# Kernel tuning notes

Measured on AMD Instinct MI355X. Metric: run time of the kernel, lower is better.

## Reference

```python
import jax, jax.numpy as jnp
import numpy as np

GAMMA = 0.9865


def setup_inputs() -> dict:
    key = jax.random.key(0)
    ks = jax.random.split(key, 6)
    B, T, DIN, D = 8, 2048, 1024, 1024
    return {
        "xq": jax.random.normal(ks[0], (B, T, DIN), dtype=jnp.float32),
        "xk": jax.random.normal(ks[1], (B, T, DIN), dtype=jnp.float32),
        "xv": jax.random.normal(ks[2], (B, T, DIN), dtype=jnp.float32),
        "Wq": jax.random.normal(ks[3], (DIN, D), dtype=jnp.float32) * (DIN ** -0.5),
        "Wk": jax.random.normal(ks[4], (DIN, D), dtype=jnp.float32) * (DIN ** -0.5),
        "Wv": jax.random.normal(ks[5], (DIN, D), dtype=jnp.float32) * (DIN ** -0.5),
    }


def reference(xq, xk, xv, Wq, Wk, Wv):
    # Dense projections (no bias)
    Q = jnp.einsum("btd,de->bte", xq, Wq)  # [B,T,D]
    K = jnp.einsum("btd,de->bte", xk, Wk)
    V = jnp.einsum("btd,de->bte", xv, Wv)

    # einsum('ib,bj->bj', K_t^T, V_t) == (sum_i K[b,t,i]) * V[b,t,:]
    ksum = jnp.sum(K, axis=-1)            # [B,T]
    u = ksum[..., None] * V               # [B,T,D]
    # recurrence starts at t=1 with s[0]=0, so u[0] never contributes
    u = u * (jnp.arange(u.shape[1]) > 0)[None, :, None]

    def step(s, u_t):
        s = s * jnp.float32(GAMMA) + u_t
        return s, s

    s0 = jnp.zeros(u.shape[::2], dtype=u.dtype)          # [B,D]
    _, S = jax.lax.scan(step, s0, jnp.swapaxes(u, 0, 1))  # S: [T,B,D]
    return Q * jnp.swapaxes(S, 0, 1)                      # [B,T,D]
```

## Files before the change

kernel.cpp:

```cpp
#include <hip/hip_runtime.h>
#include <hip/hip_bf16.h>

#define GAMMA 0.9865f

typedef __attribute__((ext_vector_type(8))) short bf16x8;
typedef __attribute__((ext_vector_type(4))) float f32x4;

static constexpr int Bb  = 8;
static constexpr int Tt  = 2048;
static constexpr int DIN = 1024;
static constexpr int Dd  = 1024;
static constexpr int Mm  = Bb * Tt;
static constexpr int CL  = 64;
static constexpr int NC  = Tt / CL;
static constexpr int NT  = DIN / 64;

__device__ __forceinline__ void gload16(const void* g, void* l) {
  __builtin_amdgcn_global_load_lds(
      (const __attribute__((address_space(1))) void*)g,
      (__attribute__((address_space(3))) void*)l, 16, 0, 0);
}

__device__ __forceinline__ void bar() {
  asm volatile("" ::: "memory");
  __builtin_amdgcn_s_barrier();
  asm volatile("" ::: "memory");
}

__global__ void wsum_kernel(const float* __restrict__ Wk, float* __restrict__ wsum) {
  int row  = blockIdx.x * 4 + (threadIdx.x >> 6);
  int lane = threadIdx.x & 63;
  const float4* rp = (const float4*)(Wk + (size_t)row * DIN);
  float s = 0.f;
#pragma unroll
  for (int i = 0; i < 4; ++i) {
    float4 v = rp[lane + i * 64];
    s += v.x + v.y + v.z + v.w;
  }
  for (int off = 32; off; off >>= 1) s += __shfl_down(s, off);
  if (lane == 0) wsum[row] = s;
}

__global__ void wt_kernel(const float* __restrict__ Wq, const float* __restrict__ Wv,
                          __hip_bfloat16* __restrict__ Wt) {
  const float* W = blockIdx.z ? Wv : Wq;
  __hip_bfloat16* outp = Wt + (size_t)blockIdx.z * DIN * Dd;
  __shared__ float tile[32][33];
  int k0 = blockIdx.x * 32, n0 = blockIdx.y * 32;
  int tx = threadIdx.x, ty = threadIdx.y;
#pragma unroll
  for (int i = 0; i < 4; ++i)
    tile[ty + i * 8][tx] = W[(size_t)(k0 + ty + i * 8) * Dd + n0 + tx];
  __syncthreads();
#pragma unroll
  for (int i = 0; i < 4; ++i)
    outp[(size_t)(n0 + ty + i * 8) * DIN + k0 + tx] =
        __float2bfloat16(tile[tx][ty + i * 8]);
}

__global__ __launch_bounds__(256) void cast_kernel(
    const float* __restrict__ xq, const float* __restrict__ xv,
    __hip_bfloat16* __restrict__ oq, __hip_bfloat16* __restrict__ ov) {
  const float* src = blockIdx.y ? xv : xq;
  __hip_bfloat16* dst = blockIdx.y ? ov : oq;
  size_t i = (size_t)blockIdx.x * 256 + threadIdx.x;
  const float4* p = (const float4*)src;
  float4 a = p[i * 2], b = p[i * 2 + 1];
  union { __hip_bfloat16 h[8]; bf16x8 v; } u;
  u.h[0] = __float2bfloat16(a.x); u.h[1] = __float2bfloat16(a.y);
  u.h[2] = __float2bfloat16(a.z); u.h[3] = __float2bfloat16(a.w);
  u.h[4] = __float2bfloat16(b.x); u.h[5] = __float2bfloat16(b.y);
  u.h[6] = __float2bfloat16(b.z); u.h[7] = __float2bfloat16(b.w);
  ((bf16x8*)dst)[i] = u.v;
}


__device__ __forceinline__ void stage_half(const __hip_bfloat16* g, char* l, int tid) {
#pragma unroll
  for (int j = 0; j < 2; ++j) {
    int c = tid + j * 512;
    int row = c >> 3, ch = c & 7;
    gload16(g + (size_t)row * DIN + ((ch ^ (row & 7)) << 3), l + c * 16);
  }
}

__device__ __forceinline__ bf16x8 lds_frag(const char* base, int row, int kc) {
  return *(const bf16x8*)(base + (((row << 3) + (kc ^ (row & 7))) << 4));
}

#define MFMA_QUAD(MLO, NLO)                                                  \
  _Pragma("unroll") for (int mi = 0; mi < 4; ++mi)                           \
  _Pragma("unroll") for (int ni = 0; ni < 2; ++ni)                           \
  _Pragma("unroll") for (int ks = 0; ks < 2; ++ks)                           \
      acc[(MLO) + mi][(NLO) + ni] = __builtin_amdgcn_mfma_f32_16x16x32_bf16( \
          a[(MLO) + mi][ks], b[(NLO) + ni][ks], acc[(MLO) + mi][(NLO) + ni], 0, 0, 0);

__global__ __launch_bounds__(512, 2) void gemm8_kernel(
    const __hip_bfloat16* __restrict__ Aq, const __hip_bfloat16* __restrict__ Av,
    const __hip_bfloat16* __restrict__ Wt,
    __hip_bfloat16* __restrict__ Qbf, __hip_bfloat16* __restrict__ Vbf) {
  extern __shared__ char lds[];

  int lin = blockIdx.x;
  int wg  = (lin & 7) * 64 + (lin >> 3);
  int z   = wg >> 8, rem = wg & 255;
  int by  = rem & 3, bx = rem >> 2;

  const __hip_bfloat16* Ab = z ? Av : Aq;
  const int m0 = bx * 256, n0 = by * 256;
  const __hip_bfloat16* Ag = Ab + (size_t)m0 * DIN;
  const __hip_bfloat16* Bg = Wt + ((size_t)z * Dd + n0) * DIN;
  __hip_bfloat16* Cc = z ? Vbf : Qbf;

  const int tid = threadIdx.x;
  const int wv = tid >> 6, lane = tid & 63;
  const int wm = (wv >> 2) * 128, wn = (wv & 3) * 64;
  const int fq = lane >> 4, fr = lane & 15;

  f32x4 acc[8][4] = {};

  stage_half(Ag,                  lds,                 tid);
  stage_half(Ag + 128 * DIN,      lds + 16384,         tid);
  stage_half(Bg,                  lds + 32768,         tid);
  stage_half(Bg + 128 * DIN,      lds + 49152,         tid);
  stage_half(Ag + 64,             lds + 65536,         tid);
  stage_half(Ag + 128 * DIN + 64, lds + 65536 + 16384, tid);
  asm volatile("s_waitcnt vmcnt(4)" ::: "memory");
  bar();

  for (int t = 0; t < NT; ++t) {
    char* buf  = lds + (t & 1) * 65536;
    char* bufN = lds + ((t + 1) & 1) * 65536;
    const char* At = buf;
    const char* Bt = buf + 32768;
    bf16x8 a[8][2], b[4][2];

#pragma unroll
    for (int mi = 0; mi < 4; ++mi)
#pragma unroll
      for (int ks = 0; ks < 2; ++ks)
        a[mi][ks] = lds_frag(At, wm + mi * 16 + fr, ks * 4 + fq);
#pragma unroll
    for (int ni = 0; ni < 2; ++ni)
#pragma unroll
      for (int ks = 0; ks < 2; ++ks)
        b[ni][ks] = lds_frag(Bt, wn + ni * 16 + fr, ks * 4 + fq);
    if (t + 1 < NT) stage_half(Bg + (size_t)(t + 1) * 64, bufN + 32768, tid);
    bar();
    __builtin_amdgcn_s_setprio(1);
    MFMA_QUAD(0, 0);
    __builtin_amdgcn_s_setprio(0);
    bar();

#pragma unroll
    for (int mi = 4; mi < 8; ++mi)
#pragma unroll
      for (int ks = 0; ks < 2; ++ks)
        a[mi][ks] = lds_frag(At, wm + mi * 16 + fr, ks * 4 + fq);
    if (t + 1 < NT)
      stage_half(Bg + 128 * DIN + (size_t)(t + 1) * 64, bufN + 49152, tid);
    bar();
    __builtin_amdgcn_s_setprio(1);
    MFMA_QUAD(4, 0);
    __builtin_amdgcn_s_setprio(0);
    bar();

#pragma unroll
    for (int ni = 2; ni < 4; ++ni)
#pragma unroll
      for (int ks = 0; ks < 2; ++ks)
        b[ni][ks] = lds_frag(Bt, wn + ni * 16 + fr, ks * 4 + fq);
    if (t + 2 < NT) stage_half(Ag + (size_t)(t + 2) * 64, buf, tid);
    bar();
    __builtin_amdgcn_s_setprio(1);
    MFMA_QUAD(0, 2);
    __builtin_amdgcn_s_setprio(0);
    bar();

    if (t + 2 < NT)
      stage_half(Ag + 128 * DIN + (size_t)(t + 2) * 64, buf + 16384, tid);
    if (t + 1 < NT) {
      if (t + 2 < NT) asm volatile("s_waitcnt vmcnt(4)" ::: "memory");
      else            asm volatile("s_waitcnt vmcnt(0)" ::: "memory");
    }
    bar();
    __builtin_amdgcn_s_setprio(1);
    MFMA_QUAD(4, 2);
    __builtin_amdgcn_s_setprio(0);
    bar();
  }

#pragma unroll
  for (int mi = 0; mi < 8; ++mi) {
#pragma unroll
    for (int ni = 0; ni < 4; ++ni) {
      f32x4 v = acc[mi][ni];
      int row = m0 + wm + mi * 16 + fq * 4;
      int col = n0 + wn + ni * 16 + fr;
#pragma unroll
      for (int j = 0; j < 4; ++j)
        Cc[(size_t)(row + j) * Dd + col] = __float2bfloat16(v[j]);
    }
  }
}

__global__ void ksum_kernel(const float* __restrict__ xk, const float* __restrict__ wsum,
                            float* __restrict__ ksum) {
  int row  = blockIdx.x * 4 + (threadIdx.x >> 6);
  int lane = threadIdx.x & 63;
  const float4* rp = (const float4*)(xk + (size_t)row * DIN);
  const float4* wp = (const float4*)wsum;
  float s = 0.f;
#pragma unroll
  for (int i = 0; i < 4; ++i) {
    float4 a = rp[lane + i * 64];
    float4 w = wp[lane + i * 64];
    s += a.x * w.x + a.y * w.y + a.z * w.z + a.w * w.w;
  }
  for (int off = 32; off; off >>= 1) s += __shfl_down(s, off);
  if (lane == 0) ksum[row] = s;
}

__global__ void scanA_kernel(const __hip_bfloat16* __restrict__ Vbf,
                             const float* __restrict__ ksum,
                             float* __restrict__ E) {
  int b = blockIdx.x, c = blockIdx.y;
  int d = blockIdx.z * 256 + threadIdx.x;
  const __hip_bfloat16* Vp = Vbf + ((size_t)(b * Tt + c * CL) * Dd) + d;
  const float* kp = ksum + b * Tt + c * CL;
  float s = 0.f;
#pragma unroll 8
  for (int t = 0; t < CL; ++t) {
    float u = kp[t] * __bfloat162float(Vp[(size_t)t * Dd]);
    if (c == 0 && t == 0) u = 0.f;
    s = s * GAMMA + u;
  }
  E[((size_t)b * NC + c) * Dd + d] = s;
}

__global__ void scanB_kernel(const float* __restrict__ E, float* __restrict__ carry,
                             float gCL) {
  int b = blockIdx.x;
  int d = blockIdx.y * 256 + threadIdx.x;
  float send = 0.f;
  for (int c = 0; c < NC; ++c) {
    size_t idx = ((size_t)b * NC + c) * Dd + d;
    float e = E[idx];
    carry[idx] = send;
    send = e + gCL * send;
  }
}

__global__ void final_kernel(const __hip_bfloat16* __restrict__ Vbf,
                             const __hip_bfloat16* __restrict__ Qbf,
                             const float* __restrict__ ksum,
                             const float* __restrict__ carry,
                             float* __restrict__ outp) {
  int b = blockIdx.x, c = blockIdx.y;
  int d = blockIdx.z * 256 + threadIdx.x;
  size_t base = ((size_t)(b * Tt + c * CL) * Dd) + d;
  float s = carry[((size_t)b * NC + c) * Dd + d];
  const float* kp = ksum + b * Tt + c * CL;
#pragma unroll 4
  for (int t = 0; t < CL; ++t) {
    float u = kp[t] * __bfloat162float(Vbf[base + (size_t)t * Dd]);
    if (c == 0 && t == 0) u = 0.f;
    s = s * GAMMA + u;
    outp[base + (size_t)t * Dd] = __bfloat162float(Qbf[base + (size_t)t * Dd]) * s;
  }
}

extern "C" void kernel_launch(void* const* d_in, const int* in_sizes, int n_in,
                              void* d_out, int out_size, void* d_ws, size_t ws_size,
                              hipStream_t stream) {
  (void)in_sizes; (void)n_in; (void)out_size; (void)ws_size;
  const float* xq = (const float*)d_in[0];
  const float* xk = (const float*)d_in[1];
  const float* xv = (const float*)d_in[2];
  const float* Wq = (const float*)d_in[3];
  const float* Wk = (const float*)d_in[4];
  const float* Wv = (const float*)d_in[5];
  float* outp = (float*)d_out;

  char* ws = (char*)d_ws;
  size_t off = 0;
  auto alloc = [&](size_t bytes) {
    char* p = ws + off;
    off += (bytes + 255) & ~(size_t)255;
    return p;
  };
  __hip_bfloat16* xq_bf = (__hip_bfloat16*)alloc((size_t)Mm * DIN * 2);
  __hip_bfloat16* xv_bf = (__hip_bfloat16*)alloc((size_t)Mm * DIN * 2);
  __hip_bfloat16* Wt    = (__hip_bfloat16*)alloc((size_t)2 * DIN * Dd * 2);
  __hip_bfloat16* Qbf   = (__hip_bfloat16*)alloc((size_t)Mm * Dd * 2);
  __hip_bfloat16* Vbf   = (__hip_bfloat16*)alloc((size_t)Mm * Dd * 2);
  float* wsum  = (float*)alloc((size_t)DIN * 4);
  float* ksum  = (float*)alloc((size_t)Mm * 4);
  float* E     = (float*)alloc((size_t)Bb * NC * Dd * 4);
  float* carry = (float*)alloc((size_t)Bb * NC * Dd * 4);

  double g = 1.0;
  for (int i = 0; i < CL; ++i) g *= (double)GAMMA;
  float gCL = (float)g;

  (void)hipFuncSetAttribute((const void*)gemm8_kernel,
                            hipFuncAttributeMaxDynamicSharedMemorySize, 131072);

  wsum_kernel<<<DIN / 4, 256, 0, stream>>>(Wk, wsum);
  wt_kernel<<<dim3(DIN / 32, Dd / 32, 2), dim3(32, 8), 0, stream>>>(Wq, Wv, Wt);
  cast_kernel<<<dim3(Mm * DIN / 8 / 256, 2), 256, 0, stream>>>(xq, xv, xq_bf, xv_bf);
  ksum_kernel<<<Mm / 4, 256, 0, stream>>>(xk, wsum, ksum);
  gemm8_kernel<<<512, 512, 131072, stream>>>(xq_bf, xv_bf, Wt, Qbf, Vbf);
  scanA_kernel<<<dim3(Bb, NC, Dd / 256), 256, 0, stream>>>(Vbf, ksum, E);
  scanB_kernel<<<dim3(Bb, Dd / 256), 256, 0, stream>>>(E, carry, gCL);
  final_kernel<<<dim3(Bb, NC, Dd / 256), 256, 0, stream>>>(Vbf, Qbf, ksum, carry, outp);
}
```

Measured before the change: 157.0 us.

## Fuse chunked scan stages into one cooperative kernel and merge weight prep kernels

Replaces the three scan kernels (chunk reduce, carry propagation, final apply) with a single cooperative kernel that uses grid-wide syncs. Each thread now handles two adjacent columns and keeps its 64 V values in registers, so V is read only once. Also merges the Wk row-sum and the weight transpose/cast into one launch. The aim is to cut launch overhead and the second V read, at the cost of 64 extra registers per thread and two grid barriers. The carry phase runs on only 4096 threads while the rest of the grid waits.

Result: slower. 236.0 us (+50.3%).

```diff
diff --git a/kernel.cpp b/kernel.cpp
--- a/kernel.cpp
+++ b/kernel.cpp
@@ -1,5 +1,6 @@
 #include <hip/hip_runtime.h>
 #include <hip/hip_bf16.h>
+#include <hip/hip_cooperative_groups.h>
 
 #define GAMMA 0.9865f
 
@@ -27,27 +28,40 @@
   asm volatile("" ::: "memory");
 }
 
-__global__ void wsum_kernel(const float* __restrict__ Wk, float* __restrict__ wsum) {
-  int row  = blockIdx.x * 4 + (threadIdx.x >> 6);
-  int lane = threadIdx.x & 63;
-  const float4* rp = (const float4*)(Wk + (size_t)row * DIN);
-  float s = 0.f;
-#pragma unroll
-  for (int i = 0; i < 4; ++i) {
-    float4 v = rp[lane + i * 64];
-    s += v.x + v.y + v.z + v.w;
-  }
-  for (int off = 32; off; off >>= 1) s += __shfl_down(s, off);
-  if (lane == 0) wsum[row] = s;
-}
-
-__global__ void wt_kernel(const float* __restrict__ Wq, const float* __restrict__ Wv,
-                          __hip_bfloat16* __restrict__ Wt) {
-  const float* W = blockIdx.z ? Wv : Wq;
-  __hip_bfloat16* outp = Wt + (size_t)blockIdx.z * DIN * Dd;
+__device__ __forceinline__ float bflo(unsigned int u) {
+  return __uint_as_float((u & 0xffffu) << 16);
+}
+__device__ __forceinline__ float bfhi(unsigned int u) {
+  return __uint_as_float(u & 0xffff0000u);
+}
+
+__global__ __launch_bounds__(256) void prep_kernel(
+    const float* __restrict__ Wq, const float* __restrict__ Wk,
+    const float* __restrict__ Wv, float* __restrict__ wsum,
+    __hip_bfloat16* __restrict__ Wt) {
+  int bid = blockIdx.x;
+  if (bid < 256) {
+    int row  = bid * 4 + (threadIdx.x >> 6);
+    int lane = threadIdx.x & 63;
+    const float4* rp = (const float4*)(Wk + (size_t)row * DIN);
+    float s = 0.f;
+#pragma unroll
+    for (int i = 0; i < 4; ++i) {
+      float4 v = rp[lane + i * 64];
+      s += v.x + v.y + v.z + v.w;
+    }
+    for (int off = 32; off; off >>= 1) s += __shfl_down(s, off);
+    if (lane == 0) wsum[row] = s;
+    return;
+  }
+  int wid = bid - 256;
+  int z = wid >> 10, rem = wid & 1023;
+  int kb = rem & 31, nb = rem >> 5;
+  const float* W = z ? Wv : Wq;
+  __hip_bfloat16* outp = Wt + (size_t)z * DIN * Dd;
   __shared__ float tile[32][33];
-  int k0 = blockIdx.x * 32, n0 = blockIdx.y * 32;
-  int tx = threadIdx.x, ty = threadIdx.y;
+  int k0 = kb * 32, n0 = nb * 32;
+  int tx = threadIdx.x & 31, ty = threadIdx.x >> 5;
 #pragma unroll
   for (int i = 0; i < 4; ++i)
     tile[ty + i * 8][tx] = W[(size_t)(k0 + ty + i * 8) * Dd + n0 + tx];
@@ -74,7 +88,6 @@
   ((bf16x8*)dst)[i] = u.v;
 }
 
-
 __device__ __forceinline__ void stage_half(const __hip_bfloat16* g, char* l, int tid) {
 #pragma unroll
   for (int j = 0; j < 2; ++j) {
@@ -221,52 +234,59 @@
   if (lane == 0) ksum[row] = s;
 }
 
-__global__ void scanA_kernel(const __hip_bfloat16* __restrict__ Vbf,
-                             const float* __restrict__ ksum,
-                             float* __restrict__ E) {
-  int b = blockIdx.x, c = blockIdx.y;
-  int d = blockIdx.z * 256 + threadIdx.x;
-  const __hip_bfloat16* Vp = Vbf + ((size_t)(b * Tt + c * CL) * Dd) + d;
+__global__ __launch_bounds__(512) void scanfused_kernel(
+    const __hip_bfloat16* __restrict__ Vbf, const __hip_bfloat16* __restrict__ Qbf,
+    const float* __restrict__ ksum, float2* __restrict__ E2,
+    float2* __restrict__ carry2, float gCL, float* __restrict__ outp) {
+  cooperative_groups::grid_group grid = cooperative_groups::this_grid();
+  int id = blockIdx.x * 512 + threadIdx.x;
+  int d2 = id & 511, c = (id >> 9) & 31, b = id >> 14;
+  const unsigned int* Vw = (const unsigned int*)Vbf;
+  size_t base = ((size_t)(b * Tt + c * CL)) * 512 + d2;
   const float* kp = ksum + b * Tt + c * CL;
-  float s = 0.f;
-#pragma unroll 8
+
+  unsigned int vs[64];
+  float s0 = 0.f, s1 = 0.f;
+#pragma unroll
   for (int t = 0; t < CL; ++t) {
-    float u = kp[t] * __bfloat162float(Vp[(size_t)t * Dd]);
-    if (c == 0 && t == 0) u = 0.f;
-    s = s * GAMMA + u;
-  }
-  E[((size_t)b * NC + c) * Dd + d] = s;
-}
-
-__global__ void scanB_kernel(const float* __restrict__ E, float* __restrict__ carry,
-                             float gCL) {
-  int b = blockIdx.x;
-  int d = blockIdx.y * 256 + threadIdx.x;
-  float send = 0.f;
-  for (int c = 0; c < NC; ++c) {
-    size_t idx = ((size_t)b * NC + c) * Dd + d;
-    float e = E[idx];
-    carry[idx] = send;
-    send = e + gCL * send;
-  }
-}
-
-__global__ void final_kernel(const __hip_bfloat16* __restrict__ Vbf,
-                             const __hip_bfloat16* __restrict__ Qbf,
-                             const float* __restrict__ ksum,
-                             const float* __restrict__ carry,
-                             float* __restrict__ outp) {
-  int b = blockIdx.x, c = blockIdx.y;
-  int d = blockIdx.z * 256 + threadIdx.x;
-  size_t base = ((size_t)(b * Tt + c * CL) * Dd) + d;
-  float s = carry[((size_t)b * NC + c) * Dd + d];
-  const float* kp = ksum + b * Tt + c * CL;
-#pragma unroll 4
+    unsigned int w = Vw[base + (size_t)t * 512];
+    vs[t] = w;
+    float kv = kp[t];
+    if (c == 0 && t == 0) kv = 0.f;
+    s0 = s0 * GAMMA + kv * bflo(w);
+    s1 = s1 * GAMMA + kv * bfhi(w);
+  }
+  E2[((size_t)b * NC + c) * 512 + d2] = make_float2(s0, s1);
+
+  grid.sync();
+
+  if (id < 4096) {
+    int bb = id >> 9, dd = id & 511;
+    float t0 = 0.f, t1 = 0.f;
+    for (int cc = 0; cc < NC; ++cc) {
+      size_t ix = ((size_t)bb * NC + cc) * 512 + dd;
+      float2 e = E2[ix];
+      carry2[ix] = make_float2(t0, t1);
+      t0 = e.x + gCL * t0;
+      t1 = e.y + gCL * t1;
+    }
+  }
+
+  grid.sync();
+
+  float2 cr = carry2[((size_t)b * NC + c) * 512 + d2];
+  s0 = cr.x; s1 = cr.y;
+  const unsigned int* Qw = (const unsigned int*)Qbf;
+  float2* Ow = (float2*)outp;
+#pragma unroll
   for (int t = 0; t < CL; ++t) {
-    float u = kp[t] * __bfloat162float(Vbf[base + (size_t)t * Dd]);
-    if (c == 0 && t == 0) u = 0.f;
-    s = s * GAMMA + u;
-    outp[base + (size_t)t * Dd] = __bfloat162float(Qbf[base + (size_t)t * Dd]) * s;
+    unsigned int w = vs[t];
+    float kv = kp[t];
+    if (c == 0 && t == 0) kv = 0.f;
+    s0 = s0 * GAMMA + kv * bflo(w);
+    s1 = s1 * GAMMA + kv * bfhi(w);
+    unsigned int qw = Qw[base + (size_t)t * 512];
+    Ow[base + (size_t)t * 512] = make_float2(bflo(qw) * s0, bfhi(qw) * s1);
   }
 }
 
@@ -294,10 +314,10 @@
   __hip_bfloat16* Wt    = (__hip_bfloat16*)alloc((size_t)2 * DIN * Dd * 2);
   __hip_bfloat16* Qbf   = (__hip_bfloat16*)alloc((size_t)Mm * Dd * 2);
   __hip_bfloat16* Vbf   = (__hip_bfloat16*)alloc((size_t)Mm * Dd * 2);
-  float* wsum  = (float*)alloc((size_t)DIN * 4);
-  float* ksum  = (float*)alloc((size_t)Mm * 4);
-  float* E     = (float*)alloc((size_t)Bb * NC * Dd * 4);
-  float* carry = (float*)alloc((size_t)Bb * NC * Dd * 4);
+  float* wsum   = (float*)alloc((size_t)DIN * 4);
+  float* ksum   = (float*)alloc((size_t)Mm * 4);
+  float2* E2    = (float2*)alloc((size_t)Bb * NC * 512 * 8);
+  float2* carry2= (float2*)alloc((size_t)Bb * NC * 512 * 8);
 
   double g = 1.0;
   for (int i = 0; i < CL; ++i) g *= (double)GAMMA;
@@ -306,12 +326,15 @@
   (void)hipFuncSetAttribute((const void*)gemm8_kernel,
                             hipFuncAttributeMaxDynamicSharedMemorySize, 131072);
 
-  wsum_kernel<<<DIN / 4, 256, 0, stream>>>(Wk, wsum);
-  wt_kernel<<<dim3(DIN / 32, Dd / 32, 2), dim3(32, 8), 0, stream>>>(Wq, Wv, Wt);
+  prep_kernel<<<256 + 2048, 256, 0, stream>>>(Wq, Wk, Wv, wsum, Wt);
   cast_kernel<<<dim3(Mm * DIN / 8 / 256, 2), 256, 0, stream>>>(xq, xv, xq_bf, xv_bf);
   ksum_kernel<<<Mm / 4, 256, 0, stream>>>(xk, wsum, ksum);
   gemm8_kernel<<<512, 512, 131072, stream>>>(xq_bf, xv_bf, Wt, Qbf, Vbf);
-  scanA_kernel<<<dim3(Bb, NC, Dd / 256), 256, 0, stream>>>(Vbf, ksum, E);
-  scanB_kernel<<<dim3(Bb, Dd / 256), 256, 0, stream>>>(E, carry, gCL);
-  final_kernel<<<dim3(Bb, NC, Dd / 256), 256, 0, stream>>>(Vbf, Qbf, ksum, carry, outp);
-}
+
+  const __hip_bfloat16* Vc = Vbf; const __hip_bfloat16* Qc = Qbf;
+  const float* kc = ksum;
+  void* cargs[] = { (void*)&Vc, (void*)&Qc, (void*)&kc, (void*)&E2,
+                    (void*)&carry2, (void*)&gCL, (void*)&outp };
+  (void)hipLaunchCooperativeKernel((const void*)scanfused_kernel,
+                                   dim3(256), dim3(512), cargs, 0, stream);
+}
```

## Fuse prep kernels and make GEMM blocks process two M tiles persistently

Applied to the files above, without the earlier changes.

The weight-sum and weight-transpose kernels are merged into one launch, and the activation cast is merged with the ksum reduction via an extra grid row. The GEMM launches 256 blocks instead of 512, and each block loops over two consecutive 256-row M tiles with the same B columns, re-staging the prologue between them. The aim is to cut launch overhead and get a single wave of blocks on the device. The cost is a serialized prologue and epilogue inside each block, plus a larger castksum grid in which many ksum blocks exit immediately.

New measurement: 173.2 us. 10.3% more time.

```diff
diff --git a/kernel.cpp b/kernel.cpp
--- a/kernel.cpp
+++ b/kernel.cpp
@@ -27,27 +27,33 @@
   asm volatile("" ::: "memory");
 }
 
-__global__ void wsum_kernel(const float* __restrict__ Wk, float* __restrict__ wsum) {
-  int row  = blockIdx.x * 4 + (threadIdx.x >> 6);
-  int lane = threadIdx.x & 63;
-  const float4* rp = (const float4*)(Wk + (size_t)row * DIN);
-  float s = 0.f;
-#pragma unroll
-  for (int i = 0; i < 4; ++i) {
-    float4 v = rp[lane + i * 64];
-    s += v.x + v.y + v.z + v.w;
-  }
-  for (int off = 32; off; off >>= 1) s += __shfl_down(s, off);
-  if (lane == 0) wsum[row] = s;
-}
-
-__global__ void wt_kernel(const float* __restrict__ Wq, const float* __restrict__ Wv,
-                          __hip_bfloat16* __restrict__ Wt) {
-  const float* W = blockIdx.z ? Wv : Wq;
-  __hip_bfloat16* outp = Wt + (size_t)blockIdx.z * DIN * Dd;
+__global__ __launch_bounds__(256) void prep_kernel(
+    const float* __restrict__ Wq, const float* __restrict__ Wk,
+    const float* __restrict__ Wv, float* __restrict__ wsum,
+    __hip_bfloat16* __restrict__ Wt) {
+  int bid = blockIdx.x;
+  if (bid < 256) {
+    int row  = bid * 4 + (threadIdx.x >> 6);
+    int lane = threadIdx.x & 63;
+    const float4* rp = (const float4*)(Wk + (size_t)row * DIN);
+    float s = 0.f;
+#pragma unroll
+    for (int i = 0; i < 4; ++i) {
+      float4 v = rp[lane + i * 64];
+      s += v.x + v.y + v.z + v.w;
+    }
+    for (int off = 32; off; off >>= 1) s += __shfl_down(s, off);
+    if (lane == 0) wsum[row] = s;
+    return;
+  }
+  int wid = bid - 256;
+  int z = wid >> 10, rem = wid & 1023;
+  int kb = rem & 31, nb = rem >> 5;
+  const float* W = z ? Wv : Wq;
+  __hip_bfloat16* outp = Wt + (size_t)z * DIN * Dd;
   __shared__ float tile[32][33];
-  int k0 = blockIdx.x * 32, n0 = blockIdx.y * 32;
-  int tx = threadIdx.x, ty = threadIdx.y;
+  int k0 = kb * 32, n0 = nb * 32;
+  int tx = threadIdx.x & 31, ty = threadIdx.x >> 5;
 #pragma unroll
   for (int i = 0; i < 4; ++i)
     tile[ty + i * 8][tx] = W[(size_t)(k0 + ty + i * 8) * Dd + n0 + tx];
@@ -58,20 +64,40 @@
         __float2bfloat16(tile[tx][ty + i * 8]);
 }
 
-__global__ __launch_bounds__(256) void cast_kernel(
-    const float* __restrict__ xq, const float* __restrict__ xv,
-    __hip_bfloat16* __restrict__ oq, __hip_bfloat16* __restrict__ ov) {
-  const float* src = blockIdx.y ? xv : xq;
-  __hip_bfloat16* dst = blockIdx.y ? ov : oq;
-  size_t i = (size_t)blockIdx.x * 256 + threadIdx.x;
-  const float4* p = (const float4*)src;
-  float4 a = p[i * 2], b = p[i * 2 + 1];
-  union { __hip_bfloat16 h[8]; bf16x8 v; } u;
-  u.h[0] = __float2bfloat16(a.x); u.h[1] = __float2bfloat16(a.y);
-  u.h[2] = __float2bfloat16(a.z); u.h[3] = __float2bfloat16(a.w);
-  u.h[4] = __float2bfloat16(b.x); u.h[5] = __float2bfloat16(b.y);
-  u.h[6] = __float2bfloat16(b.z); u.h[7] = __float2bfloat16(b.w);
-  ((bf16x8*)dst)[i] = u.v;
+__global__ __launch_bounds__(256) void castksum_kernel(
+    const float* __restrict__ xq, const float* __restrict__ xk,
+    const float* __restrict__ xv, const float* __restrict__ wsum,
+    __hip_bfloat16* __restrict__ oq, __hip_bfloat16* __restrict__ ov,
+    float* __restrict__ ksum) {
+  int y = blockIdx.y;
+  if (y < 2) {
+    const float* src = y ? xv : xq;
+    __hip_bfloat16* dst = y ? ov : oq;
+    size_t i = (size_t)blockIdx.x * 256 + threadIdx.x;
+    const float4* p = (const float4*)src;
+    float4 a = p[i * 2], b = p[i * 2 + 1];
+    union { __hip_bfloat16 h[8]; bf16x8 v; } u;
+    u.h[0] = __float2bfloat16(a.x); u.h[1] = __float2bfloat16(a.y);
+    u.h[2] = __float2bfloat16(a.z); u.h[3] = __float2bfloat16(a.w);
+    u.h[4] = __float2bfloat16(b.x); u.h[5] = __float2bfloat16(b.y);
+    u.h[6] = __float2bfloat16(b.z); u.h[7] = __float2bfloat16(b.w);
+    ((bf16x8*)dst)[i] = u.v;
+    return;
+  }
+  if (blockIdx.x >= Mm / 4) return;
+  int row  = blockIdx.x * 4 + (threadIdx.x >> 6);
+  int lane = threadIdx.x & 63;
+  const float4* rp = (const float4*)(xk + (size_t)row * DIN);
+  const float4* wp = (const float4*)wsum;
+  float s = 0.f;
+#pragma unroll
+  for (int i = 0; i < 4; ++i) {
+    float4 a = rp[lane + i * 64];
+    float4 w = wp[lane + i * 64];
+    s += a.x * w.x + a.y * w.y + a.z * w.z + a.w * w.w;
+  }
+  for (int off = 32; off; off >>= 1) s += __shfl_down(s, off);
+  if (lane == 0) ksum[row] = s;
 }
 
 
@@ -102,13 +128,12 @@
   extern __shared__ char lds[];
 
   int lin = blockIdx.x;
-  int wg  = (lin & 7) * 64 + (lin >> 3);
-  int z   = wg >> 8, rem = wg & 255;
-  int by  = rem & 3, bx = rem >> 2;
+  int wg  = (lin & 7) * 32 + (lin >> 3);
+  int z   = wg >> 7, rem = wg & 127;
+  int by  = rem & 3, bxp = rem >> 2;
 
   const __hip_bfloat16* Ab = z ? Av : Aq;
-  const int m0 = bx * 256, n0 = by * 256;
-  const __hip_bfloat16* Ag = Ab + (size_t)m0 * DIN;
+  const int n0 = by * 256;
   const __hip_bfloat16* Bg = Wt + ((size_t)z * Dd + n0) * DIN;
   __hip_bfloat16* Cc = z ? Vbf : Qbf;
 
@@ -117,108 +142,110 @@
   const int wm = (wv >> 2) * 128, wn = (wv & 3) * 64;
   const int fq = lane >> 4, fr = lane & 15;
 
-  f32x4 acc[8][4] = {};
-
-  stage_half(Ag,                  lds,                 tid);
-  stage_half(Ag + 128 * DIN,      lds + 16384,         tid);
-  stage_half(Bg,                  lds + 32768,         tid);
-  stage_half(Bg + 128 * DIN,      lds + 49152,         tid);
-  stage_half(Ag + 64,             lds + 65536,         tid);
-  stage_half(Ag + 128 * DIN + 64, lds + 65536 + 16384, tid);
-  asm volatile("s_waitcnt vmcnt(4)" ::: "memory");
-  bar();
-
-  for (int t = 0; t < NT; ++t) {
-    char* buf  = lds + (t & 1) * 65536;
-    char* bufN = lds + ((t + 1) & 1) * 65536;
-    const char* At = buf;
-    const char* Bt = buf + 32768;
-    bf16x8 a[8][2], b[4][2];
-
-#pragma unroll
-    for (int mi = 0; mi < 4; ++mi)
-#pragma unroll
-      for (int ks = 0; ks < 2; ++ks)
-        a[mi][ks] = lds_frag(At, wm + mi * 16 + fr, ks * 4 + fq);
-#pragma unroll
-    for (int ni = 0; ni < 2; ++ni)
-#pragma unroll
-      for (int ks = 0; ks < 2; ++ks)
-        b[ni][ks] = lds_frag(Bt, wn + ni * 16 + fr, ks * 4 + fq);
-    if (t + 1 < NT) stage_half(Bg + (size_t)(t + 1) * 64, bufN + 32768, tid);
+  {
+    const __hip_bfloat16* Ag = Ab + (size_t)(bxp * 2) * 256 * DIN;
+    stage_half(Ag,                  lds,                 tid);
+    stage_half(Ag + 128 * DIN,      lds + 16384,         tid);
+    stage_half(Bg,                  lds + 32768,         tid);
+    stage_half(Bg + 128 * DIN,      lds + 49152,         tid);
+    stage_half(Ag + 64,             lds + 65536,         tid);
+    stage_half(Ag + 128 * DIN + 64, lds + 65536 + 16384, tid);
+    asm volatile("s_waitcnt vmcnt(4)" ::: "memory");
     bar();
-    __builtin_amdgcn_s_setprio(1);
-    MFMA_QUAD(0, 0);
-    __builtin_amdgcn_s_setprio(0);
-    bar();
-
-#pragma unroll
-    for (int mi = 4; mi < 8; ++mi)
-#pragma unroll
-      for (int ks = 0; ks < 2; ++ks)
-        a[mi][ks] = lds_frag(At, wm + mi * 16 + fr, ks * 4 + fq);
-    if (t + 1 < NT)
-      stage_half(Bg + 128 * DIN + (size_t)(t + 1) * 64, bufN + 49152, tid);
-    bar();
-    __builtin_amdgcn_s_setprio(1);
-    MFMA_QUAD(4, 0);
-    __builtin_amdgcn_s_setprio(0);
-    bar();
-
-#pragma unroll
-    for (int ni = 2; ni < 4; ++ni)
-#pragma unroll
-      for (int ks = 0; ks < 2; ++ks)
-        b[ni][ks] = lds_frag(Bt, wn + ni * 16 + fr, ks * 4 + fq);
-    if (t + 2 < NT) stage_half(Ag + (size_t)(t + 2) * 64, buf, tid);
-    bar();
-    __builtin_amdgcn_s_setprio(1);
-    MFMA_QUAD(0, 2);
-    __builtin_amdgcn_s_setprio(0);
-    bar();
-
-    if (t + 2 < NT)
-      stage_half(Ag + 128 * DIN + (size_t)(t + 2) * 64, buf + 16384, tid);
-    if (t + 1 < NT) {
-      if (t + 2 < NT) asm volatile("s_waitcnt vmcnt(4)" ::: "memory");
-      else            asm volatile("s_waitcnt vmcnt(0)" ::: "memory");
+  }
+
+  for (int rep = 0; rep < 2; ++rep) {
+    const int m0 = (bxp * 2 + rep) * 256;
+    const __hip_bfloat16* Ag = Ab + (size_t)m0 * DIN;
+    f32x4 acc[8][4] = {};
+
+    for (int t = 0; t < NT; ++t) {
+      char* buf  = lds + (t & 1) * 65536;
+      char* bufN = lds + ((t + 1) & 1) * 65536;
+      const char* At = buf;
+      const char* Bt = buf + 32768;
+      bf16x8 a[8][2], b[4][2];
+
+#pragma unroll
+      for (int mi = 0; mi < 4; ++mi)
+#pragma unroll
+        for (int ks = 0; ks < 2; ++ks)
+          a[mi][ks] = lds_frag(At, wm + mi * 16 + fr, ks * 4 + fq);
+#pragma unroll
+      for (int ni = 0; ni < 2; ++ni)
+#pragma unroll
+        for (int ks = 0; ks < 2; ++ks)
+          b[ni][ks] = lds_frag(Bt, wn + ni * 16 + fr, ks * 4 + fq);
+      if (t + 1 < NT) stage_half(Bg + (size_t)(t + 1) * 64, bufN + 32768, tid);
+      bar();
+      __builtin_amdgcn_s_setprio(1);
+      MFMA_QUAD(0, 0);
+      __builtin_amdgcn_s_setprio(0);
+      bar();
+
+#pragma unroll
+      for (int mi = 4; mi < 8; ++mi)
+#pragma unroll
+        for (int ks = 0; ks < 2; ++ks)
+          a[mi][ks] = lds_frag(At, wm + mi * 16 + fr, ks * 4 + fq);
+      if (t + 1 < NT)
+        stage_half(Bg + 128 * DIN + (size_t)(t + 1) * 64, bufN + 49152, tid);
+      bar();
+      __builtin_amdgcn_s_setprio(1);
+      MFMA_QUAD(4, 0);
+      __builtin_amdgcn_s_setprio(0);
+      bar();
+
+#pragma unroll
+      for (int ni = 2; ni < 4; ++ni)
+#pragma unroll
+        for (int ks = 0; ks < 2; ++ks)
+          b[ni][ks] = lds_frag(Bt, wn + ni * 16 + fr, ks * 4 + fq);
+      if (t + 2 < NT) stage_half(Ag + (size_t)(t + 2) * 64, buf, tid);
+      bar();
+      __builtin_amdgcn_s_setprio(1);
+      MFMA_QUAD(0, 2);
+      __builtin_amdgcn_s_setprio(0);
+      bar();
+
+      if (t + 2 < NT)
+        stage_half(Ag + 128 * DIN + (size_t)(t + 2) * 64, buf + 16384, tid);
+      if (t + 1 < NT) {
+        if (t + 2 < NT) asm volatile("s_waitcnt vmcnt(4)" ::: "memory");
+        else            asm volatile("s_waitcnt vmcnt(0)" ::: "memory");
+      }
+      bar();
+      __builtin_amdgcn_s_setprio(1);
+      MFMA_QUAD(4, 2);
+      __builtin_amdgcn_s_setprio(0);
+      bar();
     }
-    bar();
-    __builtin_amdgcn_s_setprio(1);
-    MFMA_QUAD(4, 2);
-    __builtin_amdgcn_s_setprio(0);
-    bar();
-  }
-
-#pragma unroll
-  for (int mi = 0; mi < 8; ++mi) {
-#pragma unroll
-    for (int ni = 0; ni < 4; ++ni) {
-      f32x4 v = acc[mi][ni];
-      int row = m0 + wm + mi * 16 + fq * 4;
-      int col = n0 + wn + ni * 16 + fr;
-#pragma unroll
-      for (int j = 0; j < 4; ++j)
-        Cc[(size_t)(row + j) * Dd + col] = __float2bfloat16(v[j]);
+
+#pragma unroll
+    for (int mi = 0; mi < 8; ++mi) {
+#pragma unroll
+      for (int ni = 0; ni < 4; ++ni) {
+        f32x4 v = acc[mi][ni];
+        int row = m0 + wm + mi * 16 + fq * 4;
+        int col = n0 + wn + ni * 16 + fr;
+#pragma unroll
+        for (int j = 0; j < 4; ++j)
+          Cc[(size_t)(row + j) * Dd + col] = __float2bfloat16(v[j]);
+      }
     }
-  }
-}
-
-__global__ void ksum_kernel(const float* __restrict__ xk, const float* __restrict__ wsum,
-                            float* __restrict__ ksum) {
-  int row  = blockIdx.x * 4 + (threadIdx.x >> 6);
-  int lane = threadIdx.x & 63;
-  const float4* rp = (const float4*)(xk + (size_t)row * DIN);
-  const float4* wp = (const float4*)wsum;
-  float s = 0.f;
-#pragma unroll
-  for (int i = 0; i < 4; ++i) {
-    float4 a = rp[lane + i * 64];
-    float4 w = wp[lane + i * 64];
-    s += a.x * w.x + a.y * w.y + a.z * w.z + a.w * w.w;
-  }
-  for (int off = 32; off; off >>= 1) s += __shfl_down(s, off);
-  if (lane == 0) ksum[row] = s;
+
+    if (rep == 0) {
+      const __hip_bfloat16* Ag1 = Ab + (size_t)(m0 + 256) * DIN;
+      stage_half(Ag1,                  lds,                 tid);
+      stage_half(Ag1 + 128 * DIN,      lds + 16384,         tid);
+      stage_half(Bg,                   lds + 32768,         tid);
+      stage_half(Bg + 128 * DIN,       lds + 49152,         tid);
+      stage_half(Ag1 + 64,             lds + 65536,         tid);
+      stage_half(Ag1 + 128 * DIN + 64, lds + 65536 + 16384, tid);
+      asm volatile("s_waitcnt vmcnt(4)" ::: "memory");
+      bar();
+    }
+  }
 }
 
 __global__ void scanA_kernel(const __hip_bfloat16* __restrict__ Vbf,
@@ -306,11 +333,10 @@
   (void)hipFuncSetAttribute((const void*)gemm8_kernel,
                             hipFuncAttributeMaxDynamicSharedMemorySize, 131072);
 
-  wsum_kernel<<<DIN / 4, 256, 0, stream>>>(Wk, wsum);
-  wt_kernel<<<dim3(DIN / 32, Dd / 32, 2), dim3(32, 8), 0, stream>>>(Wq, Wv, Wt);
-  cast_kernel<<<dim3(Mm * DIN / 8 / 256, 2), 256, 0, stream>>>(xq, xv, xq_bf, xv_bf);
-  ksum_kernel<<<Mm / 4, 256, 0, stream>>>(xk, wsum, ksum);
-  gemm8_kernel<<<512, 512, 131072, stream>>>(xq_bf, xv_bf, Wt, Qbf, Vbf);
+  prep_kernel<<<256 + 2048, 256, 0, stream>>>(Wq, Wk, Wv, wsum, Wt);
+  castksum_kernel<<<dim3(Mm * DIN / 8 / 256, 3), 256, 0, stream>>>(
+      xq, xk, xv, wsum, xq_bf, xv_bf, ksum);
+  gemm8_kernel<<<256, 512, 131072, stream>>>(xq_bf, xv_bf, Wt, Qbf, Vbf);
   scanA_kernel<<<dim3(Bb, NC, Dd / 256), 256, 0, stream>>>(Vbf, ksum, E);
   scanB_kernel<<<dim3(Bb, Dd / 256), 256, 0, stream>>>(E, carry, gCL);
   final_kernel<<<dim3(Bb, NC, Dd / 256), 256, 0, stream>>>(Vbf, Qbf, ksum, carry, outp);
```
